# Kernel tuning notes

Hardware: AMD Instinct MI355X
Metric: run time of the kernel (lower is better)

The kernel has to match this reference:

```python
import jax, jax.numpy as jnp
import numpy as np

N, E, NFEAT, NHID, NCLASS = 50000, 800000, 8, 128, 112
SMOOTH = 0.5          # smoo init arg
NEG_SLOPE_ATT = 0.2   # LeakyReLU slope inside sparse attention (SpGAT convention)
NEG_SLOPE_OUT = 0.01  # F.leaky_relu default in the outer loop
EPS = 1e-16


def setup_inputs() -> dict:
    key = jax.random.key(0)
    ks = jax.random.split(key, 12)
    g = lambda k, shape, s=0.1: jax.random.normal(k, shape, dtype=jnp.float32) * s
    return {
        "x": jax.random.normal(ks[0], (N, NFEAT), dtype=jnp.float32),
        "edge_index": jax.random.randint(ks[1], (2, E), 0, N, dtype=jnp.int64) if jax.config.jax_enable_x64 else jax.random.randint(ks[1], (2, E), 0, N, dtype=jnp.int32),
        "edge_weight": jax.random.uniform(ks[2], (E,), dtype=jnp.float32),
        # ScattterAttentionLayer 1: nfeat -> nhid (weight W, attention vector a split into src/dst halves)
        "W1": g(ks[3], (NFEAT, NHID)),
        "a1_src": g(ks[4], (NHID,)),
        "a1_dst": g(ks[5], (NHID,)),
        # ScattterAttentionLayer 2: nhid -> nhid
        "W2": g(ks[6], (NHID, NHID)),
        "a2_src": g(ks[7], (NHID,)),
        "a2_dst": g(ks[8], (NHID,)),
        # shared BatchNorm1d(nhid)
        "gamma": jnp.ones((NHID,), jnp.float32),
        "beta": jnp.zeros((NHID,), jnp.float32),
        # GC_withres: nhid -> nclass
        "Wg": g(ks[9], (NHID, NCLASS)),
        "bg": jnp.zeros((NCLASS,), jnp.float32),
    }


def scatter_attention(h_in, W, a_src, a_dst, src, dst):
    """Sparse GAT-style scatter attention (SpGraphAttentionLayer math).
    score_ij = exp(-leakyrelu(a_src.h_i + a_dst.h_j)); softmax-normalized per dst node."""
    h = h_in @ W                                   # [N, F]
    f_src = h @ a_src                              # [N]
    f_dst = h @ a_dst                              # [N]
    e = jnp.exp(-jax.nn.leaky_relu(f_src[src] + f_dst[dst], NEG_SLOPE_ATT))  # [E]
    denom = jax.ops.segment_sum(e, dst, num_segments=N) + EPS                # [N]
    num = jax.ops.segment_sum(e[:, None] * h[src], dst, num_segments=N)      # [N, F]
    return num / denom[:, None]


def batchnorm(x, gamma, beta):
    mu = x.mean(axis=0)
    var = x.var(axis=0)
    return (x - mu) * jax.lax.rsqrt(var + 1e-5) * gamma + beta


def reference(x, edge_index, edge_weight, W1, a1_src, a1_dst, W2, a2_src, a2_dst, gamma, beta, Wg, bg):
    src, dst = edge_index[0], edge_index[1]
    # conv loop (nlayers=3 -> two ScattterAttentionLayer convs), shared bn1, leaky_relu; dropout=identity (eval)
    h = scatter_attention(x, W1, a1_src, a1_dst, src, dst)
    h = jax.nn.leaky_relu(batchnorm(h, gamma, beta), NEG_SLOPE_OUT)
    h = scatter_attention(h, W2, a2_src, a2_dst, src, dst)
    h = jax.nn.leaky_relu(batchnorm(h, gamma, beta), NEG_SLOPE_OUT)
    # GC_withres: spmm((smooth*A + I)/(1+smooth), h @ Wg) + bias
    support = h @ Wg                               # [N, nclass]
    w = (SMOOTH / (1.0 + SMOOTH)) * edge_weight    # [E]
    agg = jax.ops.segment_sum(w[:, None] * support[src], dst, num_segments=N)
    return agg + support / (1.0 + SMOOTH) + bg
```

## Files before the change

kernel.cpp:

```cpp
#include <hip/hip_runtime.h>
#include <hip/hip_bf16.h>

#define N_NODES 50000
#define N_EDGES 800000
#define NFEAT   8
#define NHID    128
#define NCLASS  112
#define SEG_EPS 1e-16f
#define BN_EPS  1e-5f
#define CAP     64
#define MACRO_TILES 782
#define NODE_RANGE 6250
#define FILL_CHUNK 2048
#define FILL_CHUNKS 391
#define FSFD_BLOCKS 196
#define GATH_GRID 12800
#define ATT_GRID 3200
#define ATT_IT 4
#define Y1_BLOCKS 256

typedef __hip_bfloat16 bf16;
typedef __attribute__((ext_vector_type(8))) short short8;
typedef __attribute__((ext_vector_type(4))) float f32x4;
typedef __attribute__((ext_vector_type(4))) unsigned int u32x4;

__device__ __forceinline__ float bfbits2f(unsigned int lo16) {
    union { unsigned int u; float f; } c; c.u = lo16 << 16; return c.f;
}

__device__ __forceinline__ unsigned int pack_bf2(float a, float b) {
    union { unsigned int u; bf16 h[2]; } t;
    t.h[0] = __float2bfloat16(a);
    t.h[1] = __float2bfloat16(b);
    return t.u;
}

__global__ __launch_bounds__(256)
void k_fill_fsfd(const int* __restrict__ src, const int* __restrict__ dst,
                 const float* __restrict__ ewt,
                 int* __restrict__ cnt, unsigned int* __restrict__ bucket,
                 const float* __restrict__ x, const float* __restrict__ W1,
                 const float* __restrict__ a1s, const float* __restrict__ a1d,
                 float* __restrict__ fs, float* __restrict__ fd) {
    if (blockIdx.x < FILL_CHUNKS * 8) {
        const int range = blockIdx.x & 7;
        const int chunk = blockIdx.x >> 3;
        const int lo = range * NODE_RANGE, hi = lo + NODE_RANGE;
        const int e0 = chunk * FILL_CHUNK + threadIdx.x * 8;
        if (e0 >= N_EDGES) return;
        const int4 d0 = *(const int4*)&dst[e0];
        const int4 d1 = *(const int4*)&dst[e0 + 4];
        const int dd[8] = {d0.x, d0.y, d0.z, d0.w, d1.x, d1.y, d1.z, d1.w};
#pragma unroll
        for (int i = 0; i < 8; i++) {
            int d = dd[i];
            if (d < lo || d >= hi) continue;
            int e = e0 + i;
            int slot = atomicAdd(&cnt[d], 1);
            if (slot < CAP) {
                unsigned int iw = (unsigned int)(ewt[e] * 32767.f + 0.5f);
                bucket[d * CAP + slot] = ((unsigned int)src[e] << 15) | iw;
            }
        }
        return;
    }
    __shared__ float sw[16];
    const int t = threadIdx.x, w = t >> 6, lane = t & 63;
#pragma unroll
    for (int dd = 0; dd < 4; dd++) {
        int dot = w + dd * 4;
        int k = dot & 7;
        const float* a = (dot < 8) ? a1s : a1d;
        float v = W1[k * NHID + lane] * a[lane] + W1[k * NHID + 64 + lane] * a[64 + lane];
#pragma unroll
        for (int off = 32; off > 0; off >>= 1) v += __shfl_down(v, off);
        if (lane == 0) sw[dot] = v;
    }
    __syncthreads();
    const int i = (blockIdx.x - FILL_CHUNKS * 8) * 256 + t;
    if (i < N_NODES) {
        const float4 x0 = ((const float4*)x)[i * 2];
        const float4 x1 = ((const float4*)x)[i * 2 + 1];
        fs[i] = x0.x*sw[0] + x0.y*sw[1] + x0.z*sw[2] + x0.w*sw[3]
              + x1.x*sw[4] + x1.y*sw[5] + x1.z*sw[6] + x1.w*sw[7];
        fd[i] = x0.x*sw[8] + x0.y*sw[9] + x0.z*sw[10] + x0.w*sw[11]
              + x1.x*sw[12] + x1.y*sw[13] + x1.z*sw[14] + x1.w*sw[15];
    }
}

__global__ __launch_bounds__(256)
void k_sort_gather_x(const int* __restrict__ cnt, unsigned int* __restrict__ bucket,
                     const float* __restrict__ fs, const float* __restrict__ fd,
                     const float* __restrict__ x, float* __restrict__ xaggn) {
    const int xcd = blockIdx.x & 7;
    const int wb  = blockIdx.x >> 3;
    const int ni  = wb * 4 + (threadIdx.x >> 6);
    if (ni >= NODE_RANGE) return;
    const int d = xcd * NODE_RANGE + ni;
    const int lane = threadIdx.x & 63;
    const int deg = min(cnt[d], CAP);
    unsigned int v = (lane < deg) ? bucket[d * CAP + lane] : 0xFFFFFFFFu;
#pragma unroll
    for (int k = 2; k <= 64; k <<= 1) {
#pragma unroll
        for (int s = k >> 1; s > 0; s >>= 1) {
            unsigned int o = (unsigned int)__shfl_xor((int)v, s);
            bool keepmin = ((lane & s) == 0) == ((lane & k) == 0);
            v = keepmin ? min(v, o) : max(v, o);
        }
    }
    if (lane < deg) bucket[d * CAP + lane] = v;
    const int epair = lane >> 1;
    const int half  = lane & 1;
    const float fdd = fd[d];
    float4 acc = {0.f, 0.f, 0.f, 0.f};
    float den = 0.f;
    for (int base = 0; base < deg; base += 32) {
        int e = base + epair;
        unsigned int u = (unsigned int)__shfl((int)v, e);
        if (e < deg) {
            int s = u >> 15;
            float f = fs[s] + fdd;
            float lr = f > 0.f ? f : 0.2f * f;
            float c = __expf(-lr);
            if (half == 0) den += c;
            const float4 xv = *(const float4*)&x[s * NFEAT + half * 4];
            acc.x += c * xv.x; acc.y += c * xv.y; acc.z += c * xv.z; acc.w += c * xv.w;
        }
    }
#pragma unroll
    for (int off = 2; off < 64; off <<= 1) {
        acc.x += __shfl_xor(acc.x, off);
        acc.y += __shfl_xor(acc.y, off);
        acc.z += __shfl_xor(acc.z, off);
        acc.w += __shfl_xor(acc.w, off);
        den   += __shfl_xor(den, off);
    }
    den += __shfl_xor(den, 1);
    if (lane < 2) {
        float r = 1.f / (den + SEG_EPS);
        float4 o;
        o.x = acc.x * r; o.y = acc.y * r; o.z = acc.z * r; o.w = acc.w * r;
        *(float4*)&xaggn[d * NFEAT + half * 4] = o;
    }
}

__global__ __launch_bounds__(256)
void k_y1_gemm(const float* __restrict__ xaggn, const float* __restrict__ W1,
               bf16* __restrict__ y1, float* __restrict__ Psum, float* __restrict__ Psq) {
    int t = threadIdx.x;
    int r = t >> 7, j = t & 127;
    float w[NFEAT];
#pragma unroll
    for (int k = 0; k < NFEAT; k++) w[k] = W1[k * NHID + j];
    float ls = 0.f, lq = 0.f;
    for (int row = blockIdx.x * 2 + r; row < N_NODES; row += gridDim.x * 2) {
        const float4 x0 = ((const float4*)xaggn)[row * 2];
        const float4 x1 = ((const float4*)xaggn)[row * 2 + 1];
        float v = x0.x*w[0] + x0.y*w[1] + x0.z*w[2] + x0.w*w[3]
                + x1.x*w[4] + x1.y*w[5] + x1.z*w[6] + x1.w*w[7];
        y1[(size_t)row * NHID + j] = __float2bfloat16(v);
        ls += v; lq += v * v;
    }
    __shared__ float sbuf[256];
    sbuf[t] = ls; __syncthreads();
    if (r == 0) Psum[blockIdx.x * 128 + j] = sbuf[j] + sbuf[j + 128];
    __syncthreads();
    sbuf[t] = lq; __syncthreads();
    if (r == 0) Psq[blockIdx.x * 128 + j] = sbuf[j] + sbuf[j + 128];
}

__global__ __launch_bounds__(512)
void k_bn_w2(const float* __restrict__ Psum, const float* __restrict__ Psq,
             const float* __restrict__ gamma, const float* __restrict__ beta,
             float* __restrict__ scale, float* __restrict__ shift,
             const float* __restrict__ W2,
             const float* __restrict__ as_, const float* __restrict__ ad_,
             float* __restrict__ ws_, float* __restrict__ wd_,
             const float* __restrict__ Wg,
             bf16* __restrict__ W2t, bf16* __restrict__ Wgt) {
    const int t = threadIdx.x;
    if (blockIdx.x == 0) {
        int j = t & 127;
        int g = t >> 7;
        float s = 0.f, q = 0.f;
#pragma unroll 8
        for (int b = g * 64; b < g * 64 + 64; b++) {
            s += Psum[b * 128 + j];
            q += Psq[b * 128 + j];
        }
        __shared__ float Ls[4][128], Lq[4][128];
        Ls[g][j] = s; Lq[g][j] = q;
        __syncthreads();
        if (g == 0) {
            float st = ((Ls[0][j] + Ls[1][j]) + Ls[2][j]) + Ls[3][j];
            float qt = ((Lq[0][j] + Lq[1][j]) + Lq[2][j]) + Lq[3][j];
            float mu = st * (1.f / N_NODES);
            float var = qt * (1.f / N_NODES) - mu * mu;
            float rs = rsqrtf(var + BN_EPS);
            float ga = gamma[j];
            scale[j] = rs * ga;
            shift[j] = beta[j] - mu * rs * ga;
        }
        return;
    }
    if (blockIdx.x < 33) {
        const int k = (blockIdx.x - 1) * 4 + (t >> 7);
        const int n = t & 127;
        float wv = W2[k * NHID + n];
        float vs = wv * as_[n], vd = wv * ad_[n];
#pragma unroll
        for (int off = 32; off > 0; off >>= 1) { vs += __shfl_down(vs, off); vd += __shfl_down(vd, off); }
        __shared__ float ps[8], pd[8];
        const int wid = t >> 6;
        if ((t & 63) == 0) { ps[wid] = vs; pd[wid] = vd; }
        __syncthreads();
        if ((t & 127) == 0) { ws_[k] = ps[wid] + ps[wid + 1]; wd_[k] = pd[wid] + pd[wid + 1]; }
        return;
    }
    if (blockIdx.x < 49) {
        const int n = (blockIdx.x - 33) * 8 + (t >> 6);
        const int k2 = (t & 63) * 2;
        float v0 = W2[k2 * NHID + n];
        float v1 = W2[(k2 + 1) * NHID + n];
        *(unsigned int*)&W2t[n * 128 + k2] = pack_bf2(v0, v1);
        return;
    }
    const int n = (blockIdx.x - 49) * 8 + (t >> 6);
    const int k2 = (t & 63) * 2;
    float v0 = Wg[k2 * NCLASS + n];
    float v1 = Wg[(k2 + 1) * NCLASS + n];
    *(unsigned int*)&Wgt[n * 128 + k2] = pack_bf2(v0, v1);
}

__global__ __launch_bounds__(256)
void k_reduce_a(const float* __restrict__ Psum, const float* __restrict__ Psq,
                int nIn, int chunk,
                float* __restrict__ Qsum, float* __restrict__ Qsq) {
    int j = threadIdx.x & 127;
    int h = threadIdx.x >> 7;
    int u = blockIdx.x * 2 + h;
    int b0 = u * chunk, b1 = min(b0 + chunk, nIn);
    float s = 0.f, q = 0.f;
#pragma unroll 8
    for (int b = b0; b < b1; b++) {
        s += Psum[b * 128 + j];
        q += Psq[b * 128 + j];
    }
    Qsum[u * 128 + j] = s;
    Qsq[u * 128 + j] = q;
}

__global__ __launch_bounds__(512)
void k_reduce_b(const float* __restrict__ Qsum, const float* __restrict__ Qsq,
                const float* __restrict__ gamma, const float* __restrict__ beta,
                float* __restrict__ scale, float* __restrict__ shift) {
    int j = threadIdx.x & 127;
    int g = threadIdx.x >> 7;
    float s = 0.f, q = 0.f;
#pragma unroll
    for (int u = g * 8; u < g * 8 + 8; u++) {
        s += Qsum[u * 128 + j];
        q += Qsq[u * 128 + j];
    }
    __shared__ float Ls[4][128], Lq[4][128];
    Ls[g][j] = s; Lq[g][j] = q;
    __syncthreads();
    if (g == 0) {
        float st = ((Ls[0][j] + Ls[1][j]) + Ls[2][j]) + Ls[3][j];
        float qt = ((Lq[0][j] + Lq[1][j]) + Lq[2][j]) + Lq[3][j];
        float mu = st * (1.f / N_NODES);
        float var = qt * (1.f / N_NODES) - mu * mu;
        float rs = rsqrtf(var + BN_EPS);
        float ga = gamma[j];
        scale[j] = rs * ga;
        shift[j] = beta[j] - mu * rs * ga;
    }
}

template<int NCV, bool ATT>
__global__ __launch_bounds__(256)
void k_gemm_mfma(const bf16* __restrict__ Yin,
                 const float* __restrict__ scale, const float* __restrict__ shift,
                 const bf16* __restrict__ Wt_g,
                 bf16* __restrict__ hout,
                 const float* __restrict__ w2s, const float* __restrict__ w2d,
                 float* __restrict__ fs, float* __restrict__ fd) {
    constexpr int NT = NCV / 16;
    __shared__ bf16 Wt[NCV * 136];
    __shared__ float scb[128], shb[128];
    const int t = threadIdx.x;
    for (int idx = t; idx < NCV * 16; idx += 256) {
        int n = idx >> 4, c = idx & 15;
        *(u32x4*)&Wt[n * 136 + c * 8] = *(const u32x4*)&Wt_g[n * 128 + c * 8];
    }
    if (t < 128) { scb[t] = scale[t]; shb[t] = shift[t]; }
    const int lane = t & 63;
    const int m16 = lane & 15;
    const int g = lane >> 4;
    const int rg = t >> 6;
    short8 attb[4];
    if constexpr (ATT) {
#pragma unroll
        for (int kk = 0; kk < 4; kk++) {
            union { short8 s; unsigned int u[4]; } pk;
            if (m16 < 2) {
                const float* wv = (m16 == 0) ? w2s : w2d;
                const float4 f0 = *(const float4*)&wv[kk * 32 + g * 8];
                const float4 f1 = *(const float4*)&wv[kk * 32 + g * 8 + 4];
                pk.u[0] = pack_bf2(f0.x, f0.y);
                pk.u[1] = pack_bf2(f0.z, f0.w);
                pk.u[2] = pack_bf2(f1.x, f1.y);
                pk.u[3] = pack_bf2(f1.z, f1.w);
            } else {
                pk.u[0] = pk.u[1] = pk.u[2] = pk.u[3] = 0u;
            }
            attb[kk] = pk.s;
        }
    }
    __syncthreads();

    const int row0 = blockIdx.x * 64;
    const int arow = row0 + rg * 16 + m16;
    const bool rok = arow < N_NODES;
    f32x4 acc[NT];
#pragma unroll
    for (int c = 0; c < NT; c++) acc[c] = (f32x4){0.f, 0.f, 0.f, 0.f};
    f32x4 accA = (f32x4){0.f, 0.f, 0.f, 0.f};
#pragma unroll
    for (int kk = 0; kk < 4; kk++) {
        u32x4 u4 = rok
            ? *(const u32x4*)&((const unsigned int*)Yin)[(size_t)arow * 64 + kk * 16 + g * 4]
            : (u32x4){0u, 0u, 0u, 0u};
        const float4 s0 = *(const float4*)&scb[kk * 32 + g * 8];
        const float4 s1 = *(const float4*)&scb[kk * 32 + g * 8 + 4];
        const float4 h0 = *(const float4*)&shb[kk * 32 + g * 8];
        const float4 h1 = *(const float4*)&shb[kk * 32 + g * 8 + 4];
        const float scv[8] = {s0.x, s0.y, s0.z, s0.w, s1.x, s1.y, s1.z, s1.w};
        const float shv[8] = {h0.x, h0.y, h0.z, h0.w, h1.x, h1.y, h1.z, h1.w};
        union { short8 s; unsigned int u[4]; } A;
#pragma unroll
        for (int fq = 0; fq < 4; fq++) {
            unsigned int u = u4[fq];
            float v0 = bfbits2f(u & 0xFFFF) * scv[2*fq]   + shv[2*fq];   v0 = v0 > 0.f ? v0 : 0.01f * v0;
            float v1 = bfbits2f(u >> 16)    * scv[2*fq+1] + shv[2*fq+1]; v1 = v1 > 0.f ? v1 : 0.01f * v1;
            A.u[fq] = pack_bf2(v0, v1);
        }
#pragma unroll
        for (int c = 0; c < NT; c++) {
            short8 bfr = *(const short8*)&Wt[(c * 16 + m16) * 136 + kk * 32 + g * 8];
            acc[c] = __builtin_amdgcn_mfma_f32_16x16x32_bf16(A.s, bfr, acc[c], 0, 0, 0);
        }
        if constexpr (ATT)
            accA = __builtin_amdgcn_mfma_f32_16x16x32_bf16(A.s, attb[kk], accA, 0, 0, 0);
    }
    const int orow = row0 + rg * 16 + g * 4;
#pragma unroll
    for (int c = 0; c < NT; c++) {
#pragma unroll
        for (int r = 0; r < 4; r++) {
            int grow = orow + r;
            if (grow < N_NODES)
                hout[(size_t)grow * 128 + c * 16 + m16] = __float2bfloat16(acc[c][r]);
        }
    }
    if constexpr (ATT) {
        if (m16 < 2) {
            float* o = (m16 == 0) ? fs : fd;
#pragma unroll
            for (int r = 0; r < 4; r++) {
                int grow = orow + r;
                if (grow < N_NODES) o[grow] = accA[r];
            }
        }
    }
}

__global__ __launch_bounds__(256)
void k_gather_attn_bf(const int* __restrict__ cnt, const unsigned int* __restrict__ bucket,
                      const float* __restrict__ fs, const float* __restrict__ fd,
                      const bf16* __restrict__ h, bf16* __restrict__ y,
                      float* __restrict__ Psum, float* __restrict__ Psq) {
    const int xcd = blockIdx.x & 7;
    const int wb  = blockIdx.x >> 3;
    const int t = threadIdx.x;
    const int q = t >> 6;
    const int lane = t & 63;
    const int grp = lane >> 4;
    const int l = lane & 15;
    __shared__ int s_idx[4][CAP];
    __shared__ float s_e[4][CAP];
    __shared__ float sred[4][16][8];
    float ls[8], lq[8];
#pragma unroll
    for (int i = 0; i < 8; i++) { ls[i] = 0.f; lq[i] = 0.f; }

    for (int it = 0; it < ATT_IT; it++) {
        const int ni = (wb + it * 400) * 4 + q;
        if (ni >= NODE_RANGE) continue;
        const int d = xcd * NODE_RANGE + ni;
        const int deg = min(cnt[d], CAP);
        const float fdd = fd[d];
        if (lane < deg) {
            int s = bucket[d * CAP + lane] >> 15;
            float f = fs[s] + fdd;
            float lr = f > 0.f ? f : 0.2f * f;
            s_idx[q][lane] = s;
            s_e[q][lane] = __expf(-lr);
        }
        float a[8];
#pragma unroll
        for (int i = 0; i < 8; i++) a[i] = 0.f;
        float den = 0.f;
#pragma unroll 4
        for (int base = 0; base < deg; base += 4) {
            int k = base + grp;
            bool ev = k < deg;
            int kk = ev ? k : 0;
            float e = ev ? s_e[q][kk] : 0.f;
            int sidx = s_idx[q][kk];
            u32x4 u4 = *(const u32x4*)&((const unsigned int*)h)[(size_t)sidx * 64 + l * 4];
            den += e;
#pragma unroll
            for (int fq = 0; fq < 4; fq++) {
                unsigned int u = u4[fq];
                a[2*fq]   += e * bfbits2f(u & 0xFFFF);
                a[2*fq+1] += e * bfbits2f(u >> 16);
            }
        }
#pragma unroll
        for (int off = 16; off < 64; off <<= 1) {
#pragma unroll
            for (int i = 0; i < 8; i++) a[i] += __shfl_xor(a[i], off);
            den += __shfl_xor(den, off);
        }
        float r = 1.f / (den + SEG_EPS);
        if (lane < 16) {
            u32x4 pk;
#pragma unroll
            for (int fq = 0; fq < 4; fq++) {
                float v0 = a[2*fq] * r, v1 = a[2*fq+1] * r;
                pk[fq] = pack_bf2(v0, v1);
                ls[2*fq] += v0;   lq[2*fq] += v0 * v0;
                ls[2*fq+1] += v1; lq[2*fq+1] += v1 * v1;
            }
            *(u32x4*)&((unsigned int*)y)[(size_t)d * 64 + l * 4] = pk;
        }
    }
    if (lane < 16) {
#pragma unroll
        for (int i = 0; i < 8; i++) sred[q][l][i] = ls[i];
    }
    __syncthreads();
    if (t < 128) {
        int l16 = t >> 3, i8 = t & 7;
        Psum[blockIdx.x * 128 + t] =
            ((sred[0][l16][i8] + sred[1][l16][i8]) + sred[2][l16][i8]) + sred[3][l16][i8];
    }
    __syncthreads();
    if (lane < 16) {
#pragma unroll
        for (int i = 0; i < 8; i++) sred[q][l][i] = lq[i];
    }
    __syncthreads();
    if (t < 128) {
        int l16 = t >> 3, i8 = t & 7;
        Psq[blockIdx.x * 128 + t] =
            ((sred[0][l16][i8] + sred[1][l16][i8]) + sred[2][l16][i8]) + sred[3][l16][i8];
    }
}

__global__ __launch_bounds__(256)
void k_gather_out_bf(const int* __restrict__ cnt, const unsigned int* __restrict__ bucket,
                     const bf16* __restrict__ sup, const float* __restrict__ bg,
                     float* __restrict__ out) {
    const int xcd = blockIdx.x & 7;
    const int wb  = blockIdx.x >> 3;
    const int ni  = wb * 4 + (threadIdx.x >> 6);
    if (ni >= NODE_RANGE) return;
    const int d = xcd * NODE_RANGE + ni;
    const int t = threadIdx.x;
    const int q = t >> 6;
    const int lane = t & 63;
    const int grp = lane >> 4;
    const int l = lane & 15;
    __shared__ int s_idx[4][CAP];
    __shared__ float s_w[4][CAP];
    const int deg = min(cnt[d], CAP);
    if (lane < deg) {
        unsigned int b = bucket[d * CAP + lane];
        s_idx[q][lane] = b >> 15;
        s_w[q][lane] = (float)(b & 0x7FFF) * (1.f / (32767.f * 3.f));
    }
    float a[8];
#pragma unroll
    for (int i = 0; i < 8; i++) a[i] = 0.f;
#pragma unroll 4
    for (int base = 0; base < deg; base += 4) {
        int k = base + grp;
        bool ev = k < deg;
        int kk = ev ? k : 0;
        float w = ev ? s_w[q][kk] : 0.f;
        int sidx = s_idx[q][kk];
        u32x4 u4 = *(const u32x4*)&((const unsigned int*)sup)[(size_t)sidx * 64 + l * 4];
#pragma unroll
        for (int fq = 0; fq < 4; fq++) {
            unsigned int u = u4[fq];
            a[2*fq]   += w * bfbits2f(u & 0xFFFF);
            a[2*fq+1] += w * bfbits2f(u >> 16);
        }
    }
#pragma unroll
    for (int off = 16; off < 64; off <<= 1) {
#pragma unroll
        for (int i = 0; i < 8; i++) a[i] += __shfl_xor(a[i], off);
    }
    if (l < 14) {
        u32x4 us = *(const u32x4*)&((const unsigned int*)sup)[(size_t)d * 64 + l * 4];
        const float4 b0 = *(const float4*)&bg[l * 8];
        const float4 b1 = *(const float4*)&bg[l * 8 + 4];
        float4 o0, o1;
        o0.x = a[0] + bfbits2f(us[0] & 0xFFFF) * (2.f/3.f) + b0.x;
        o0.y = a[1] + bfbits2f(us[0] >> 16)    * (2.f/3.f) + b0.y;
        o0.z = a[2] + bfbits2f(us[1] & 0xFFFF) * (2.f/3.f) + b0.z;
        o0.w = a[3] + bfbits2f(us[1] >> 16)    * (2.f/3.f) + b0.w;
        o1.x = a[4] + bfbits2f(us[2] & 0xFFFF) * (2.f/3.f) + b1.x;
        o1.y = a[5] + bfbits2f(us[2] >> 16)    * (2.f/3.f) + b1.y;
        o1.z = a[6] + bfbits2f(us[3] & 0xFFFF) * (2.f/3.f) + b1.z;
        o1.w = a[7] + bfbits2f(us[3] >> 16)    * (2.f/3.f) + b1.w;
        *(float4*)&out[(size_t)d * NCLASS + l * 8]     = o0;
        *(float4*)&out[(size_t)d * NCLASS + l * 8 + 4] = o1;
    }
}

extern "C" void kernel_launch(void* const* d_in, const int* in_sizes, int n_in,
                              void* d_out, int out_size, void* d_ws, size_t ws_size,
                              hipStream_t stream) {
    const float* x    = (const float*)d_in[0];
    const int*   ei   = (const int*)d_in[1];
    const float* ewt  = (const float*)d_in[2];
    const float* W1   = (const float*)d_in[3];
    const float* a1s  = (const float*)d_in[4];
    const float* a1d  = (const float*)d_in[5];
    const float* W2   = (const float*)d_in[6];
    const float* a2s  = (const float*)d_in[7];
    const float* a2d  = (const float*)d_in[8];
    const float* gam  = (const float*)d_in[9];
    const float* bet  = (const float*)d_in[10];
    const float* Wg   = (const float*)d_in[11];
    const float* bg   = (const float*)d_in[12];
    float* out = (float*)d_out;

    const int* src = ei;
    const int* dst = ei + N_EDGES;

    float* ws    = (float*)d_ws;
    bf16*  Yb    = (bf16*)ws;
    bf16*  Hb    = (bf16*)(ws + 3203072);
    unsigned int* bucket = (unsigned int*)(ws + 6403072);
    float* xagg  = ws + 9603072;
    float* fs    = ws + 10003072;
    float* fd    = ws + 10053072;
    int*   cnt   = (int*)(ws + 10103072);
    float* scale = ws + 10153072;
    float* shift = scale + 128;
    float* w2s   = shift + 128;
    float* w2d   = w2s + 128;
    float* Psum  = ws + 10153600;
    float* Psq   = Psum + 409600;
    float* Qsum  = Psq + 409600;
    float* Qsq   = Qsum + 4096;
    bf16*  W2t   = (bf16*)(ws + 10980992);
    bf16*  Wgt   = W2t + 16384;

    hipMemsetAsync(cnt, 0, (size_t)N_NODES * 4, stream);
    k_fill_fsfd<<<FILL_CHUNKS * 8 + FSFD_BLOCKS, 256, 0, stream>>>(
        src, dst, ewt, cnt, bucket, x, W1, a1s, a1d, fs, fd);

    k_sort_gather_x<<<GATH_GRID, 256, 0, stream>>>(cnt, bucket, fs, fd, x, xagg);
    k_y1_gemm<<<Y1_BLOCKS, 256, 0, stream>>>(xagg, W1, Yb, Psum, Psq);
    k_bn_w2<<<63, 512, 0, stream>>>(Psum, Psq, gam, bet, scale, shift,
                                    W2, a2s, a2d, w2s, w2d, Wg, W2t, Wgt);

    k_gemm_mfma<128, true><<<MACRO_TILES, 256, 0, stream>>>(Yb, scale, shift, W2t, Hb,
                                                            w2s, w2d, fs, fd);
    k_gather_attn_bf<<<ATT_GRID, 256, 0, stream>>>(cnt, bucket, fs, fd, Hb, Yb,
                                                   Psum, Psq);
    k_reduce_a<<<16, 256, 0, stream>>>(Psum, Psq, ATT_GRID, 100, Qsum, Qsq);
    k_reduce_b<<<1, 512, 0, stream>>>(Qsum, Qsq, gam, bet, scale, shift);

    k_gemm_mfma<112, false><<<MACRO_TILES, 256, 0, stream>>>(Yb, scale, shift, Wgt, Hb,
                                                             nullptr, nullptr, nullptr, nullptr);
    k_gather_out_bf<<<GATH_GRID, 256, 0, stream>>>(cnt, bucket, Hb, bg, out);
}
```

Baseline: 299.2 us.

## Fuse layer-1 gather with W1 projection and move weight prep into fill kernel

```diff
diff --git a/kernel.cpp b/kernel.cpp
--- a/kernel.cpp
+++ b/kernel.cpp
@@ -17,12 +17,19 @@
 #define GATH_GRID 12800
 #define ATT_GRID 3200
 #define ATT_IT 4
-#define Y1_BLOCKS 256
+
+#define FILLB (FILL_CHUNKS * 8)
+#define FSFD0 FILLB
+#define W2P0  (FSFD0 + FSFD_BLOCKS)
+#define W2T0  (W2P0 + 64)
+#define WGT0  (W2T0 + 32)
+#define GRID_FILL (WGT0 + 28)
 
 typedef __hip_bfloat16 bf16;
 typedef __attribute__((ext_vector_type(8))) short short8;
 typedef __attribute__((ext_vector_type(4))) float f32x4;
 typedef __attribute__((ext_vector_type(4))) unsigned int u32x4;
+typedef __attribute__((ext_vector_type(4))) int i32x4;
 
 __device__ __forceinline__ float bfbits2f(unsigned int lo16) {
     union { unsigned int u; float f; } c; c.u = lo16 << 16; return c.f;
@@ -41,15 +48,23 @@
                  int* __restrict__ cnt, unsigned int* __restrict__ bucket,
                  const float* __restrict__ x, const float* __restrict__ W1,
                  const float* __restrict__ a1s, const float* __restrict__ a1d,
-                 float* __restrict__ fs, float* __restrict__ fd) {
-    if (blockIdx.x < FILL_CHUNKS * 8) {
+                 float* __restrict__ fs, float* __restrict__ fd,
+                 const float* __restrict__ W2,
+                 const float* __restrict__ a2s, const float* __restrict__ a2d,
+                 float* __restrict__ w2s, float* __restrict__ w2d,
+                 const float* __restrict__ Wg,
+                 bf16* __restrict__ W2t, bf16* __restrict__ Wgt) {
+    __shared__ float sw[16];
+    __shared__ float ps[4], pd[4];
+    const int t = threadIdx.x;
+    if (blockIdx.x < FILLB) {
         const int range = blockIdx.x & 7;
         const int chunk = blockIdx.x >> 3;
         const int lo = range * NODE_RANGE, hi = lo + NODE_RANGE;
-        const int e0 = chunk * FILL_CHUNK + threadIdx.x * 8;
+        const int e0 = chunk * FILL_CHUNK + t * 8;
         if (e0 >= N_EDGES) return;
-        const int4 d0 = *(const int4*)&dst[e0];
-        const int4 d1 = *(const int4*)&dst[e0 + 4];
+        const i32x4 d0 = __builtin_nontemporal_load((const i32x4*)&dst[e0]);
+        const i32x4 d1 = __builtin_nontemporal_load((const i32x4*)&dst[e0 + 4]);
         const int dd[8] = {d0.x, d0.y, d0.z, d0.w, d1.x, d1.y, d1.z, d1.w};
 #pragma unroll
         for (int i = 0; i < 8; i++) {
@@ -58,179 +73,162 @@
             int e = e0 + i;
             int slot = atomicAdd(&cnt[d], 1);
             if (slot < CAP) {
-                unsigned int iw = (unsigned int)(ewt[e] * 32767.f + 0.5f);
-                bucket[d * CAP + slot] = ((unsigned int)src[e] << 15) | iw;
+                float w = __builtin_nontemporal_load(&ewt[e]);
+                int   s = __builtin_nontemporal_load(&src[e]);
+                unsigned int iw = (unsigned int)(w * 32767.f + 0.5f);
+                bucket[d * CAP + slot] = ((unsigned int)s << 15) | iw;
             }
         }
         return;
     }
-    __shared__ float sw[16];
-    const int t = threadIdx.x, w = t >> 6, lane = t & 63;
-#pragma unroll
-    for (int dd = 0; dd < 4; dd++) {
-        int dot = w + dd * 4;
-        int k = dot & 7;
-        const float* a = (dot < 8) ? a1s : a1d;
-        float v = W1[k * NHID + lane] * a[lane] + W1[k * NHID + 64 + lane] * a[64 + lane];
-#pragma unroll
-        for (int off = 32; off > 0; off >>= 1) v += __shfl_down(v, off);
-        if (lane == 0) sw[dot] = v;
-    }
-    __syncthreads();
-    const int i = (blockIdx.x - FILL_CHUNKS * 8) * 256 + t;
-    if (i < N_NODES) {
-        const float4 x0 = ((const float4*)x)[i * 2];
-        const float4 x1 = ((const float4*)x)[i * 2 + 1];
-        fs[i] = x0.x*sw[0] + x0.y*sw[1] + x0.z*sw[2] + x0.w*sw[3]
-              + x1.x*sw[4] + x1.y*sw[5] + x1.z*sw[6] + x1.w*sw[7];
-        fd[i] = x0.x*sw[8] + x0.y*sw[9] + x0.z*sw[10] + x0.w*sw[11]
-              + x1.x*sw[12] + x1.y*sw[13] + x1.z*sw[14] + x1.w*sw[15];
-    }
-}
-
-__global__ __launch_bounds__(256)
-void k_sort_gather_x(const int* __restrict__ cnt, unsigned int* __restrict__ bucket,
-                     const float* __restrict__ fs, const float* __restrict__ fd,
-                     const float* __restrict__ x, float* __restrict__ xaggn) {
-    const int xcd = blockIdx.x & 7;
-    const int wb  = blockIdx.x >> 3;
-    const int ni  = wb * 4 + (threadIdx.x >> 6);
-    if (ni >= NODE_RANGE) return;
-    const int d = xcd * NODE_RANGE + ni;
-    const int lane = threadIdx.x & 63;
-    const int deg = min(cnt[d], CAP);
-    unsigned int v = (lane < deg) ? bucket[d * CAP + lane] : 0xFFFFFFFFu;
-#pragma unroll
-    for (int k = 2; k <= 64; k <<= 1) {
-#pragma unroll
-        for (int s = k >> 1; s > 0; s >>= 1) {
-            unsigned int o = (unsigned int)__shfl_xor((int)v, s);
-            bool keepmin = ((lane & s) == 0) == ((lane & k) == 0);
-            v = keepmin ? min(v, o) : max(v, o);
-        }
-    }
-    if (lane < deg) bucket[d * CAP + lane] = v;
-    const int epair = lane >> 1;
-    const int half  = lane & 1;
-    const float fdd = fd[d];
-    float4 acc = {0.f, 0.f, 0.f, 0.f};
-    float den = 0.f;
-    for (int base = 0; base < deg; base += 32) {
-        int e = base + epair;
-        unsigned int u = (unsigned int)__shfl((int)v, e);
-        if (e < deg) {
-            int s = u >> 15;
-            float f = fs[s] + fdd;
-            float lr = f > 0.f ? f : 0.2f * f;
-            float c = __expf(-lr);
-            if (half == 0) den += c;
-            const float4 xv = *(const float4*)&x[s * NFEAT + half * 4];
-            acc.x += c * xv.x; acc.y += c * xv.y; acc.z += c * xv.z; acc.w += c * xv.w;
-        }
-    }
-#pragma unroll
-    for (int off = 2; off < 64; off <<= 1) {
-        acc.x += __shfl_xor(acc.x, off);
-        acc.y += __shfl_xor(acc.y, off);
-        acc.z += __shfl_xor(acc.z, off);
-        acc.w += __shfl_xor(acc.w, off);
-        den   += __shfl_xor(den, off);
-    }
-    den += __shfl_xor(den, 1);
-    if (lane < 2) {
-        float r = 1.f / (den + SEG_EPS);
-        float4 o;
-        o.x = acc.x * r; o.y = acc.y * r; o.z = acc.z * r; o.w = acc.w * r;
-        *(float4*)&xaggn[d * NFEAT + half * 4] = o;
-    }
-}
-
-__global__ __launch_bounds__(256)
-void k_y1_gemm(const float* __restrict__ xaggn, const float* __restrict__ W1,
-               bf16* __restrict__ y1, float* __restrict__ Psum, float* __restrict__ Psq) {
-    int t = threadIdx.x;
-    int r = t >> 7, j = t & 127;
-    float w[NFEAT];
-#pragma unroll
-    for (int k = 0; k < NFEAT; k++) w[k] = W1[k * NHID + j];
-    float ls = 0.f, lq = 0.f;
-    for (int row = blockIdx.x * 2 + r; row < N_NODES; row += gridDim.x * 2) {
-        const float4 x0 = ((const float4*)xaggn)[row * 2];
-        const float4 x1 = ((const float4*)xaggn)[row * 2 + 1];
-        float v = x0.x*w[0] + x0.y*w[1] + x0.z*w[2] + x0.w*w[3]
-                + x1.x*w[4] + x1.y*w[5] + x1.z*w[6] + x1.w*w[7];
-        y1[(size_t)row * NHID + j] = __float2bfloat16(v);
-        ls += v; lq += v * v;
-    }
-    __shared__ float sbuf[256];
-    sbuf[t] = ls; __syncthreads();
-    if (r == 0) Psum[blockIdx.x * 128 + j] = sbuf[j] + sbuf[j + 128];
-    __syncthreads();
-    sbuf[t] = lq; __syncthreads();
-    if (r == 0) Psq[blockIdx.x * 128 + j] = sbuf[j] + sbuf[j + 128];
-}
-
-__global__ __launch_bounds__(512)
-void k_bn_w2(const float* __restrict__ Psum, const float* __restrict__ Psq,
-             const float* __restrict__ gamma, const float* __restrict__ beta,
-             float* __restrict__ scale, float* __restrict__ shift,
-             const float* __restrict__ W2,
-             const float* __restrict__ as_, const float* __restrict__ ad_,
-             float* __restrict__ ws_, float* __restrict__ wd_,
-             const float* __restrict__ Wg,
-             bf16* __restrict__ W2t, bf16* __restrict__ Wgt) {
-    const int t = threadIdx.x;
-    if (blockIdx.x == 0) {
-        int j = t & 127;
-        int g = t >> 7;
-        float s = 0.f, q = 0.f;
-#pragma unroll 8
-        for (int b = g * 64; b < g * 64 + 64; b++) {
-            s += Psum[b * 128 + j];
-            q += Psq[b * 128 + j];
-        }
-        __shared__ float Ls[4][128], Lq[4][128];
-        Ls[g][j] = s; Lq[g][j] = q;
+    if (blockIdx.x < W2P0) {
+        const int w = t >> 6, lane = t & 63;
+#pragma unroll
+        for (int dd = 0; dd < 4; dd++) {
+            int dot = w + dd * 4;
+            int k = dot & 7;
+            const float* a = (dot < 8) ? a1s : a1d;
+            float v = W1[k * NHID + lane] * a[lane] + W1[k * NHID + 64 + lane] * a[64 + lane];
+#pragma unroll
+            for (int off = 32; off > 0; off >>= 1) v += __shfl_down(v, off);
+            if (lane == 0) sw[dot] = v;
+        }
         __syncthreads();
-        if (g == 0) {
-            float st = ((Ls[0][j] + Ls[1][j]) + Ls[2][j]) + Ls[3][j];
-            float qt = ((Lq[0][j] + Lq[1][j]) + Lq[2][j]) + Lq[3][j];
-            float mu = st * (1.f / N_NODES);
-            float var = qt * (1.f / N_NODES) - mu * mu;
-            float rs = rsqrtf(var + BN_EPS);
-            float ga = gamma[j];
-            scale[j] = rs * ga;
-            shift[j] = beta[j] - mu * rs * ga;
+        const int i = (blockIdx.x - FSFD0) * 256 + t;
+        if (i < N_NODES) {
+            const float4 x0 = ((const float4*)x)[i * 2];
+            const float4 x1 = ((const float4*)x)[i * 2 + 1];
+            fs[i] = x0.x*sw[0] + x0.y*sw[1] + x0.z*sw[2] + x0.w*sw[3]
+                  + x1.x*sw[4] + x1.y*sw[5] + x1.z*sw[6] + x1.w*sw[7];
+            fd[i] = x0.x*sw[8] + x0.y*sw[9] + x0.z*sw[10] + x0.w*sw[11]
+                  + x1.x*sw[12] + x1.y*sw[13] + x1.z*sw[14] + x1.w*sw[15];
         }
         return;
     }
-    if (blockIdx.x < 33) {
-        const int k = (blockIdx.x - 1) * 4 + (t >> 7);
+    if (blockIdx.x < W2T0) {
+        const int k = (blockIdx.x - W2P0) * 2 + (t >> 7);
         const int n = t & 127;
         float wv = W2[k * NHID + n];
-        float vs = wv * as_[n], vd = wv * ad_[n];
+        float vs = wv * a2s[n], vd = wv * a2d[n];
 #pragma unroll
         for (int off = 32; off > 0; off >>= 1) { vs += __shfl_down(vs, off); vd += __shfl_down(vd, off); }
-        __shared__ float ps[8], pd[8];
         const int wid = t >> 6;
         if ((t & 63) == 0) { ps[wid] = vs; pd[wid] = vd; }
         __syncthreads();
-        if ((t & 127) == 0) { ws_[k] = ps[wid] + ps[wid + 1]; wd_[k] = pd[wid] + pd[wid + 1]; }
+        if ((t & 127) == 0) { w2s[k] = ps[wid] + ps[wid + 1]; w2d[k] = pd[wid] + pd[wid + 1]; }
         return;
     }
-    if (blockIdx.x < 49) {
-        const int n = (blockIdx.x - 33) * 8 + (t >> 6);
+    if (blockIdx.x < WGT0) {
+        const int n = (blockIdx.x - W2T0) * 4 + (t >> 6);
         const int k2 = (t & 63) * 2;
-        float v0 = W2[k2 * NHID + n];
-        float v1 = W2[(k2 + 1) * NHID + n];
-        *(unsigned int*)&W2t[n * 128 + k2] = pack_bf2(v0, v1);
+        *(unsigned int*)&W2t[n * 128 + k2] = pack_bf2(W2[k2 * NHID + n], W2[(k2 + 1) * NHID + n]);
         return;
     }
-    const int n = (blockIdx.x - 49) * 8 + (t >> 6);
+    const int n = (blockIdx.x - WGT0) * 4 + (t >> 6);
     const int k2 = (t & 63) * 2;
-    float v0 = Wg[k2 * NCLASS + n];
-    float v1 = Wg[(k2 + 1) * NCLASS + n];
-    *(unsigned int*)&Wgt[n * 128 + k2] = pack_bf2(v0, v1);
+    *(unsigned int*)&Wgt[n * 128 + k2] = pack_bf2(Wg[k2 * NCLASS + n], Wg[(k2 + 1) * NCLASS + n]);
+}
+
+__global__ __launch_bounds__(256)
+void k_sort_gather_y1(const int* __restrict__ cnt, unsigned int* __restrict__ bucket,
+                      const float* __restrict__ fs, const float* __restrict__ fd,
+                      const float* __restrict__ x, const float* __restrict__ W1,
+                      bf16* __restrict__ y1,
+                      float* __restrict__ Psum, float* __restrict__ Psq) {
+    const int xcd = blockIdx.x & 7;
+    const int wb  = blockIdx.x >> 3;
+    const int t = threadIdx.x;
+    const int q = t >> 6;
+    const int lane = t & 63;
+    const int ni = wb * 4 + q;
+    const bool nok = ni < NODE_RANGE;
+    const int d = xcd * NODE_RANGE + ni;
+    float w1c0[8], w1c1[8];
+#pragma unroll
+    for (int k = 0; k < 8; k++) {
+        const float2 wv = *(const float2*)&W1[k * NHID + 2 * lane];
+        w1c0[k] = wv.x; w1c1[k] = wv.y;
+    }
+    float v0 = 0.f, v1 = 0.f;
+    if (nok) {
+        const int deg = min(cnt[d], CAP);
+        unsigned int v = (lane < deg) ? bucket[d * CAP + lane] : 0xFFFFFFFFu;
+#pragma unroll
+        for (int k = 2; k <= 64; k <<= 1) {
+#pragma unroll
+            for (int s = k >> 1; s > 0; s >>= 1) {
+                unsigned int o = (unsigned int)__shfl_xor((int)v, s);
+                bool keepmin = ((lane & s) == 0) == ((lane & k) == 0);
+                v = keepmin ? min(v, o) : max(v, o);
+            }
+        }
+        if (lane < deg) bucket[d * CAP + lane] = v;
+        const int epair = lane >> 1;
+        const int half  = lane & 1;
+        const float fdd = fd[d];
+        float4 acc = {0.f, 0.f, 0.f, 0.f};
+        float den = 0.f;
+        for (int base = 0; base < deg; base += 32) {
+            int e = base + epair;
+            unsigned int u = (unsigned int)__shfl((int)v, e);
+            if (e < deg) {
+                int s = u >> 15;
+                float f = fs[s] + fdd;
+                float lr = f > 0.f ? f : 0.2f * f;
+                float c = __expf(-lr);
+                if (half == 0) den += c;
+                const float4 xv = *(const float4*)&x[s * NFEAT + half * 4];
+                acc.x += c * xv.x; acc.y += c * xv.y; acc.z += c * xv.z; acc.w += c * xv.w;
+            }
+        }
+#pragma unroll
+        for (int off = 2; off < 64; off <<= 1) {
+            acc.x += __shfl_xor(acc.x, off);
+            acc.y += __shfl_xor(acc.y, off);
+            acc.z += __shfl_xor(acc.z, off);
+            acc.w += __shfl_xor(acc.w, off);
+            den   += __shfl_xor(den, off);
+        }
+        den += __shfl_xor(den, 1);
+        float4 oth;
+        oth.x = __shfl_xor(acc.x, 1);
+        oth.y = __shfl_xor(acc.y, 1);
+        oth.z = __shfl_xor(acc.z, 1);
+        oth.w = __shfl_xor(acc.w, 1);
+        const float r = 1.f / (den + SEG_EPS);
+        float xa[8];
+        if ((lane & 1) == 0) {
+            xa[0]=acc.x*r; xa[1]=acc.y*r; xa[2]=acc.z*r; xa[3]=acc.w*r;
+            xa[4]=oth.x*r; xa[5]=oth.y*r; xa[6]=oth.z*r; xa[7]=oth.w*r;
+        } else {
+            xa[0]=oth.x*r; xa[1]=oth.y*r; xa[2]=oth.z*r; xa[3]=oth.w*r;
+            xa[4]=acc.x*r; xa[5]=acc.y*r; xa[6]=acc.z*r; xa[7]=acc.w*r;
+        }
+#pragma unroll
+        for (int k = 0; k < 8; k++) {
+            v0 += xa[k] * w1c0[k];
+            v1 += xa[k] * w1c1[k];
+        }
+        ((unsigned int*)y1)[(size_t)d * 64 + lane] = pack_bf2(v0, v1);
+    }
+    __shared__ float sred[4][64][2];
+    sred[q][lane][0] = nok ? v0 : 0.f;
+    sred[q][lane][1] = nok ? v1 : 0.f;
+    __syncthreads();
+    if (t < 128) {
+        int ln = t >> 1, cp = t & 1;
+        Psum[blockIdx.x * 128 + t] =
+            ((sred[0][ln][cp] + sred[1][ln][cp]) + sred[2][ln][cp]) + sred[3][ln][cp];
+    }
+    __syncthreads();
+    sred[q][lane][0] = nok ? v0 * v0 : 0.f;
+    sred[q][lane][1] = nok ? v1 * v1 : 0.f;
+    __syncthreads();
+    if (t < 128) {
+        int ln = t >> 1, cp = t & 1;
+        Psq[blockIdx.x * 128 + t] =
+            ((sred[0][ln][cp] + sred[1][ln][cp]) + sred[2][ln][cp]) + sred[3][ln][cp];
+    }
 }
 
 __global__ __launch_bounds__(256)
@@ -558,7 +556,6 @@
     bf16*  Yb    = (bf16*)ws;
     bf16*  Hb    = (bf16*)(ws + 3203072);
     unsigned int* bucket = (unsigned int*)(ws + 6403072);
-    float* xagg  = ws + 9603072;
     float* fs    = ws + 10003072;
     float* fd    = ws + 10053072;
     int*   cnt   = (int*)(ws + 10103072);
@@ -567,20 +564,21 @@
     float* w2s   = shift + 128;
     float* w2d   = w2s + 128;
     float* Psum  = ws + 10153600;
-    float* Psq   = Psum + 409600;
-    float* Qsum  = Psq + 409600;
+    float* Psq   = Psum + 1638400;
+    float* Qsum  = Psq + 1638400;
     float* Qsq   = Qsum + 4096;
-    bf16*  W2t   = (bf16*)(ws + 10980992);
+    bf16*  W2t   = (bf16*)(Qsq + 4096);
     bf16*  Wgt   = W2t + 16384;
 
     hipMemsetAsync(cnt, 0, (size_t)N_NODES * 4, stream);
-    k_fill_fsfd<<<FILL_CHUNKS * 8 + FSFD_BLOCKS, 256, 0, stream>>>(
-        src, dst, ewt, cnt, bucket, x, W1, a1s, a1d, fs, fd);
-
-    k_sort_gather_x<<<GATH_GRID, 256, 0, stream>>>(cnt, bucket, fs, fd, x, xagg);
-    k_y1_gemm<<<Y1_BLOCKS, 256, 0, stream>>>(xagg, W1, Yb, Psum, Psq);
-    k_bn_w2<<<63, 512, 0, stream>>>(Psum, Psq, gam, bet, scale, shift,
-                                    W2, a2s, a2d, w2s, w2d, Wg, W2t, Wgt);
+    k_fill_fsfd<<<GRID_FILL, 256, 0, stream>>>(
+        src, dst, ewt, cnt, bucket, x, W1, a1s, a1d, fs, fd,
+        W2, a2s, a2d, w2s, w2d, Wg, W2t, Wgt);
+
+    k_sort_gather_y1<<<GATH_GRID, 256, 0, stream>>>(cnt, bucket, fs, fd, x, W1,
+                                                    Yb, Psum, Psq);
+    k_reduce_a<<<16, 256, 0, stream>>>(Psum, Psq, GATH_GRID, 400, Qsum, Qsq);
+    k_reduce_b<<<1, 512, 0, stream>>>(Qsum, Qsq, gam, bet, scale, shift);
 
     k_gemm_mfma<128, true><<<MACRO_TILES, 256, 0, stream>>>(Yb, scale, shift, W2t, Hb,
                                                             w2s, w2d, fs, fd);
```

Measured after the change: 295.8 us. Within noise of the previous version (-1.1%).
